# Performance work log

Measured on AMD Instinct MI355X. Metric: run time of the kernel, lower is better.

The kernel has to match this reference:

```python
import jax, jax.numpy as jnp
import numpy as np
from jax import lax

R = 3                      # blob_r
S = 2 * R + 1              # 7: maxpool / neighborhood kernel size
THRESH = 0.997
PS_XY = 0.1                # vs_xy
PS_Z = 0.02                # vs_z
ZMIN = -2.0                # zrange[0]
K_PEAKS = 131072           # static upper bound replacing torch.nonzero

_offs = np.arange(S)
_gz, _gy, _gx = np.meshgrid(_offs, _offs, _offs, indexing='ij')  # patch axis order [z,y,x]
GZ = jnp.asarray(_gz.ravel(), dtype=jnp.int32)
GY = jnp.asarray(_gy.ravel(), dtype=jnp.int32)
GX = jnp.asarray(_gx.ravel(), dtype=jnp.int32)
# centroid filters: offsets -r..r along the matching patch axis (matches torch meshgrid layout)
FZ = jnp.asarray((_gz.ravel() - R).astype(np.float32))
FY = jnp.asarray((_gy.ravel() - R).astype(np.float32))
FX = jnp.asarray((_gx.ravel() - R).astype(np.float32))


def setup_inputs() -> dict:
    key = jax.random.key(0)
    pred_vol = jax.random.uniform(key, (1, 1, 128, 512, 512), dtype=jnp.float32)
    return {"pred_vol": pred_vol, "max_peaks": K_PEAKS}


def _forward(pred_vol, max_peaks):
    vol = pred_vol[0, 0]                               # [D,H,W]
    D, H, W = vol.shape
    thr = jnp.where(vol > THRESH, vol, 0.0)
    # MaxPool3d(kernel=2r+1, stride=1, padding=r) == SAME max window (pad with -inf)
    mp = lax.reduce_window(thr, -jnp.inf, lax.max, (S, S, S), (1, 1, 1), [(R, R)] * 3)
    conf = jnp.where((mp > 0.0) & (mp == thr), mp, 0.0)  # local maxima above threshold
    # fixed-size peak extraction (replaces torch.nonzero); zero-valued entries are padding
    vals, idx = lax.top_k(conf.reshape(-1), max_peaks)   # [K], [K]
    z = idx // (H * W)
    y = (idx % (H * W)) // W
    x = idx % W
    padv = jnp.pad(vol, R)                               # ConstantPad3d(r, 0)
    # gather (2r+1)^3 neighborhoods around each peak: [K, S^3]
    patches = padv[z[:, None] + GZ[None, :], y[:, None] + GY[None, :], x[:, None] + GX[None, :]]
    s0 = patches.sum(axis=1)                             # conv3d with ones filter == conf_rec sum
    xloc = jnp.einsum('kp,p->k', patches, FX) / s0
    yloc = jnp.einsum('kp,p->k', patches, FY) / s0
    zloc = jnp.einsum('kp,p->k', patches, FZ) / s0
    xf = x.astype(jnp.float32)
    yf = y.astype(jnp.float32)
    zf = z.astype(jnp.float32)
    xrec = (xf + xloc - (W - 1) / 2.0) * PS_XY
    yrec = (yf + yloc - (H - 1) / 2.0) * PS_XY
    zrec = (zf + zloc + 0.5) * PS_Z + ZMIN
    valid = vals > 0.0
    xyz = jnp.where(valid[:, None], jnp.stack((xrec, yrec, zrec), axis=1), 0.0)  # [K,3]
    out = jnp.concatenate([xyz, vals[:, None]], axis=1)  # [K,4] = (x,y,z,conf), padded rows are 0
    return out, valid


def reference(pred_vol, max_peaks):
    return _forward(pred_vol, max_peaks)
```

## Files before the change

### kernel.cpp

```cpp
#include <hip/hip_runtime.h>

#define DD 128
#define HH 512
#define WW 512
#define NVOX (DD*HH*WW)
#define THRESHV 0.997f
#define KPEAKS 131072
#define PEAK_CAP (1u<<18)
#define NBINS 65536


__global__ void k_init(unsigned* counters, unsigned* hist) {
    unsigned t = blockIdx.x * 1024u + threadIdx.x;
    if (t < 64) counters[t] = 0u;
    if (t < NBINS) hist[t] = 0u;
}

__global__ __launch_bounds__(512, 4)
void k_find(const float4* __restrict__ vol4, const float* __restrict__ vol,
            unsigned* counters, unsigned* hist,
            unsigned long long* keys, float4* psums) {
    __shared__ float4 tile[2][2048];
    __shared__ unsigned lcnt, pcnt, lbase;
    __shared__ unsigned cidx[384];
    __shared__ unsigned long long lbuf[192];
    __shared__ float4 sbuf[192];
    if (threadIdx.x == 0) { lcnt = 0; pcnt = 0; }
    __syncthreads();

    unsigned t = threadIdx.x;
    unsigned lane = t & 63u;
    unsigned w = t >> 6;
    unsigned blockBase4 = blockIdx.x * 4096u;
    int dz = (int)lane / 7, dy = (int)lane - dz * 7;

    auto dma = [&](unsigned s) {
#pragma unroll
        for (unsigned i = 0; i < 4; i++) {
            unsigned f = i * 512u + w * 64u;
            const float4* gp = vol4 + blockBase4 + s * 2048u + f + lane;
            __builtin_amdgcn_global_load_lds(
                (const __attribute__((address_space(1))) unsigned int*)gp,
                (__attribute__((address_space(3))) unsigned int*)(&tile[s][f]),
                16, 0, 0);
        }
    };

    auto scan = [&](unsigned s) {
        unsigned m = 0u;
        float4 v[4];
#pragma unroll
        for (unsigned i = 0; i < 4; i++) v[i] = tile[s][i * 512u + t];
#pragma unroll
        for (unsigned i = 0; i < 4; i++) {
            m |= (v[i].x > THRESHV ? 1u : 0u) << (4 * i);
            m |= (v[i].y > THRESHV ? 1u : 0u) << (4 * i + 1);
            m |= (v[i].z > THRESHV ? 1u : 0u) << (4 * i + 2);
            m |= (v[i].w > THRESHV ? 1u : 0u) << (4 * i + 3);
        }
        unsigned sbase4 = blockBase4 + s * 2048u;
        while (m) {
            int b = __ffs(m) - 1;
            m &= m - 1u;
            unsigned f4 = sbase4 + (unsigned)(b >> 2) * 512u + t;
            cidx[atomicAdd(&lcnt, 1u) & 383u] = f4 * 4u + (unsigned)(b & 3);
        }
    };

    auto verify = [&](unsigned n) {
        for (unsigned base = w * 2u; base < n; base += 16u) {
            bool has2 = (base + 1u < n);
            unsigned idxA = cidx[base];
            unsigned idxB = has2 ? cidx[base + 1u] : idxA;
            int zA = idxA >> 18, yA = (idxA >> 9) & 511, xA = idxA & 511;
            int zB = idxB >> 18, yB = (idxB >> 9) & 511, xB = idxB & 511;
            int nzA = zA + dz - 3, nyA = yA + dy - 3;
            int nzB = zB + dz - 3, nyB = yB + dy - 3;
            bool rowokA = (lane < 49) && ((unsigned)nzA < DD) && ((unsigned)nyA < HH);
            bool rowokB = (lane < 49) && ((unsigned)nzB < DD) && ((unsigned)nyB < HH);
            size_t rbA = rowokA ? (((size_t)(unsigned)nzA << 18) | ((size_t)(unsigned)nyA << 9))
                                : (((size_t)zA << 18) | ((size_t)yA << 9));
            size_t rbB = rowokB ? (((size_t)(unsigned)nzB << 18) | ((size_t)(unsigned)nyB << 9))
                                : (((size_t)zB << 18) | ((size_t)yB << 9));
            float rvA[7], rvB[7];
            bool intAB = (xA >= 3) && (xA <= WW - 4) && (xB >= 3) && (xB <= WW - 4);
            if (intAB) {
                float4 fA0 = *(const float4*)(vol + rbA + (unsigned)(xA - 3));
                float4 fA1 = *(const float4*)(vol + rbA + (unsigned)(xA + 1));
                float4 fB0 = *(const float4*)(vol + rbB + (unsigned)(xB - 3));
                float4 fB1 = *(const float4*)(vol + rbB + (unsigned)(xB + 1));
                rvA[0] = fA0.x; rvA[1] = fA0.y; rvA[2] = fA0.z; rvA[3] = fA0.w;
                rvA[4] = fA1.x; rvA[5] = fA1.y; rvA[6] = fA1.z;
                rvB[0] = fB0.x; rvB[1] = fB0.y; rvB[2] = fB0.z; rvB[3] = fB0.w;
                rvB[4] = fB1.x; rvB[5] = fB1.y; rvB[6] = fB1.z;
            } else {
#pragma unroll
                for (int d = 0; d < 7; d++) {
                    int nxA = xA + d - 3;
                    bool okA = (unsigned)nxA < WW;
                    float va = vol[rbA + (unsigned)(okA ? nxA : xA)];
                    rvA[d] = okA ? va : 0.f;
                    int nxB = xB + d - 3;
                    bool okB = (unsigned)nxB < WW;
                    float vb = vol[rbB + (unsigned)(okB ? nxB : xB)];
                    rvB[d] = okB ? vb : 0.f;
                }
            }
            if (!rowokA) {
#pragma unroll
                for (int d = 0; d < 7; d++) rvA[d] = 0.f;
            }
            if (!rowokB) {
#pragma unroll
                for (int d = 0; d < 7; d++) rvB[d] = 0.f;
            }
            float centerA = __shfl(rvA[3], 24);
            float centerB = __shfl(rvB[3], 24);

            {
                bool kill = false;
                float s0r = 0.f, sxr = 0.f;
#pragma unroll
                for (int d = 0; d < 7; d++) {
                    kill |= rvA[d] > centerA;
                    s0r += rvA[d];
                    sxr += rvA[d] * (float)(d - 3);
                }
                if (!__any(kill)) {
                    float s0 = s0r, sx = sxr;
                    float sy = s0r * (float)(dy - 3);
                    float sz = s0r * (float)(dz - 3);
                    for (int off = 32; off; off >>= 1) {
                        s0 += __shfl_down(s0, off);
                        sx += __shfl_down(sx, off);
                        sy += __shfl_down(sy, off);
                        sz += __shfl_down(sz, off);
                    }
                    if (lane == 0) {
                        unsigned bits = __float_as_uint(centerA);
                        atomicAdd(&hist[(~bits) & 0xFFFFu], 1u);
                        unsigned li = atomicAdd(&pcnt, 1u);
                        if (li < 192u) {
                            lbuf[li] = ((unsigned long long)bits << 32) | idxA;
                            sbuf[li] = make_float4(s0, sx, sy, sz);
                        }
                    }
                }
            }
            if (has2) {
                bool kill = false;
                float s0r = 0.f, sxr = 0.f;
#pragma unroll
                for (int d = 0; d < 7; d++) {
                    kill |= rvB[d] > centerB;
                    s0r += rvB[d];
                    sxr += rvB[d] * (float)(d - 3);
                }
                if (!__any(kill)) {
                    float s0 = s0r, sx = sxr;
                    float sy = s0r * (float)(dy - 3);
                    float sz = s0r * (float)(dz - 3);
                    for (int off = 32; off; off >>= 1) {
                        s0 += __shfl_down(s0, off);
                        sx += __shfl_down(sx, off);
                        sy += __shfl_down(sy, off);
                        sz += __shfl_down(sz, off);
                    }
                    if (lane == 0) {
                        unsigned bits = __float_as_uint(centerB);
                        atomicAdd(&hist[(~bits) & 0xFFFFu], 1u);
                        unsigned li = atomicAdd(&pcnt, 1u);
                        if (li < 192u) {
                            lbuf[li] = ((unsigned long long)bits << 32) | idxB;
                            sbuf[li] = make_float4(s0, sx, sy, sz);
                        }
                    }
                }
            }
        }
    };

    dma(0u);
    __builtin_amdgcn_s_waitcnt(0);
    __syncthreads();
    scan(0u);
    __syncthreads();
    unsigned n0 = lcnt > 384u ? 384u : lcnt;

    dma(1u);
    verify(n0);
    __syncthreads();
    if (t == 0) lcnt = 0;
    __syncthreads();

    scan(1u);
    __syncthreads();
    unsigned n1 = lcnt > 384u ? 384u : lcnt;
    verify(n1);

    __syncthreads();
    if (threadIdx.x == 0) lbase = atomicAdd(&counters[1], pcnt);
    __syncthreads();
    unsigned np = pcnt > 192u ? 192u : pcnt;
    for (unsigned i = threadIdx.x; i < np; i += 512u) {
        unsigned p = lbase + i;
        if (p < PEAK_CAP) { keys[p] = lbuf[i]; psums[p] = sbuf[i]; }
    }
}

__global__ void k_scan_a(const unsigned* __restrict__ hist,
                         unsigned* __restrict__ cursor,
                         unsigned* __restrict__ blocksum) {
    __shared__ unsigned sc[256];
    unsigned t = threadIdx.x, b = blockIdx.x;
    unsigned h = hist[b * 256u + t];
    sc[t] = h;
    __syncthreads();
    for (unsigned off = 1u; off < 256u; off <<= 1) {
        unsigned v = (t >= off) ? sc[t - off] : 0u;
        __syncthreads();
        sc[t] += v;
        __syncthreads();
    }
    cursor[b * 256u + t] = sc[t] - h;
    if (t == 255u) blocksum[b] = sc[255];
}

__global__ void k_scatter(const unsigned* __restrict__ counters,
                          const unsigned long long* __restrict__ keys,
                          const unsigned* __restrict__ blocksum,
                          unsigned* cursor, unsigned long long* sorted,
                          unsigned* sslot,
                          float4* __restrict__ out, float* __restrict__ valid) {
    __shared__ unsigned bs[256];
    unsigned t = threadIdx.x;
    if (t < 256u) bs[t] = blocksum[t];
    __syncthreads();
    for (unsigned off = 1u; off < 256u; off <<= 1) {
        unsigned v = (t < 256u && t >= off) ? bs[t - off] : 0u;
        __syncthreads();
        if (t < 256u) bs[t] += v;
        __syncthreads();
    }
    unsigned np = counters[1]; if (np > PEAK_CAP) np = PEAK_CAP;
    unsigned g = blockIdx.x * 1024u + t;
    if (g < np) {
        unsigned long long key = keys[g];
        unsigned bits = (unsigned)(key >> 32);
        unsigned bin = (~bits) & 0xFFFFu;
        unsigned c = bin >> 8;
        unsigned base_c = (c > 0u) ? bs[c - 1u] : 0u;
        unsigned pos = base_c + atomicAdd(&cursor[bin], 1u);
        if (pos < PEAK_CAP) { sorted[pos] = key; sslot[pos] = g; }
    } else if (g < KPEAKS) {
        out[g] = make_float4(0.f, 0.f, 0.f, 0.f);
        valid[g] = 0.f;
    }
}

__global__ void k_finish(const unsigned* __restrict__ counters,
                         const unsigned long long* __restrict__ sorted,
                         const unsigned* __restrict__ sslot,
                         const float4* __restrict__ psums,
                         float4* __restrict__ out, float* __restrict__ valid) {
    unsigned np = counters[1]; if (np > PEAK_CAP) np = PEAK_CAP;
    unsigned t = blockIdx.x * 1024u + threadIdx.x;
    if (t >= np) return;
    unsigned long long key = sorted[t];
    unsigned bits = (unsigned)(key >> 32);
    unsigned s = t;
    while (s > 0 && (unsigned)(sorted[s - 1] >> 32) == bits) s--;
    unsigned myidx = (unsigned)key;
    unsigned rank = 0, e = s;
    while (e < np) {
        unsigned long long k2 = sorted[e];
        if ((unsigned)(k2 >> 32) != bits) break;
        if ((unsigned)k2 < myidx) rank++;
        e++;
    }
    unsigned row = s + rank;
    if (row >= KPEAKS) return;
    unsigned idx = myidx;
    int z = idx >> 18, y = (idx >> 9) & 511, x = idx & 511;
    float4 ps = psums[sslot[t]];
    float val = __uint_as_float(bits);
    float xloc = ps.y / ps.x, yloc = ps.z / ps.x, zloc = ps.w / ps.x;
    float xr = ((float)x + xloc - (float)(WW - 1) * 0.5f) * 0.1f;
    float yr = ((float)y + yloc - (float)(HH - 1) * 0.5f) * 0.1f;
    float zr = ((float)z + zloc + 0.5f) * 0.02f - 2.0f;
    out[row] = make_float4(xr, yr, zr, val);
    valid[row] = 1.f;
}

extern "C" void kernel_launch(void* const* d_in, const int* in_sizes, int n_in,
                              void* d_out, int out_size, void* d_ws, size_t ws_size,
                              hipStream_t stream) {
    const float* vol = (const float*)d_in[0];

    char* w = (char*)d_ws;
    unsigned* counters = (unsigned*)w;
    unsigned* hist     = (unsigned*)(w + 1024);
    unsigned* cursor   = (unsigned*)(w + 1024 + NBINS * 4);
    char* w2 = w + 1024 + 2 * NBINS * 4;
    unsigned long long* keys   = (unsigned long long*)w2;
    unsigned long long* sorted = keys + PEAK_CAP;
    unsigned* sslot = (unsigned*)(sorted + PEAK_CAP);
    float4*   psums = (float4*)(sslot + PEAK_CAP);
    unsigned* blocksum = (unsigned*)(psums + PEAK_CAP);

    float* out_rows = (float*)d_out;
    float* valid = out_rows + (size_t)KPEAKS * 4;

    k_init<<<NBINS / 1024, 1024, 0, stream>>>(counters, hist);
    k_find<<<NVOX / 16384, 512, 0, stream>>>((const float4*)vol, vol, counters, hist, keys, psums);
    k_scan_a<<<256, 256, 0, stream>>>(hist, cursor, blocksum);
    k_scatter<<<PEAK_CAP / 1024, 1024, 0, stream>>>(counters, keys, blocksum, cursor,
                                                    sorted, sslot,
                                                    (float4*)out_rows, valid);
    k_finish<<<PEAK_CAP / 1024, 1024, 0, stream>>>(counters, sorted, sslot, psums,
                                                   (float4*)out_rows, valid);
}
```

Measured before the change: 252.6 us.

## Replace double-buffered LDS DMA with direct register loads, halve block work

k_find no longer copies the volume into a 64KB double-buffered LDS tile with global_load_lds. Each thread now loads its four float4 values straight into registers. Each block covers half as many voxels, so the grid doubles and launch bounds go from 4 to 8 blocks per CU. This drops the LDS footprint and the staging synchronisation so more waves are resident to hide memory latency, but it gives up the overlap between the second tile's DMA and the first tile's verify pass.

```diff
diff --git a/kernel.cpp b/kernel.cpp
--- a/kernel.cpp
+++ b/kernel.cpp
@@ -16,11 +16,10 @@
     if (t < NBINS) hist[t] = 0u;
 }
 
-__global__ __launch_bounds__(512, 4)
+__global__ __launch_bounds__(512, 8)
 void k_find(const float4* __restrict__ vol4, const float* __restrict__ vol,
             unsigned* counters, unsigned* hist,
             unsigned long long* keys, float4* psums) {
-    __shared__ float4 tile[2][2048];
     __shared__ unsigned lcnt, pcnt, lbase;
     __shared__ unsigned cidx[384];
     __shared__ unsigned long long lbuf[192];
@@ -31,173 +30,151 @@
     unsigned t = threadIdx.x;
     unsigned lane = t & 63u;
     unsigned w = t >> 6;
-    unsigned blockBase4 = blockIdx.x * 4096u;
+    unsigned blockBase4 = blockIdx.x * 2048u;
+
+    unsigned b4 = blockBase4 + t;
+    float4 a0 = vol4[b4];
+    float4 a1 = vol4[b4 + 512u];
+    float4 a2 = vol4[b4 + 1024u];
+    float4 a3 = vol4[b4 + 1536u];
+    __builtin_amdgcn_sched_barrier(0);
+    unsigned m = 0u;
+    m |= (a0.x > THRESHV ? 1u : 0u);
+    m |= (a0.y > THRESHV ? 2u : 0u);
+    m |= (a0.z > THRESHV ? 4u : 0u);
+    m |= (a0.w > THRESHV ? 8u : 0u);
+    m |= (a1.x > THRESHV ? 16u : 0u);
+    m |= (a1.y > THRESHV ? 32u : 0u);
+    m |= (a1.z > THRESHV ? 64u : 0u);
+    m |= (a1.w > THRESHV ? 128u : 0u);
+    m |= (a2.x > THRESHV ? 256u : 0u);
+    m |= (a2.y > THRESHV ? 512u : 0u);
+    m |= (a2.z > THRESHV ? 1024u : 0u);
+    m |= (a2.w > THRESHV ? 2048u : 0u);
+    m |= (a3.x > THRESHV ? 4096u : 0u);
+    m |= (a3.y > THRESHV ? 8192u : 0u);
+    m |= (a3.z > THRESHV ? 16384u : 0u);
+    m |= (a3.w > THRESHV ? 32768u : 0u);
+    while (m) {
+        int b = __ffs(m) - 1;
+        m &= m - 1u;
+        unsigned f4 = blockBase4 + (unsigned)(b >> 2) * 512u + t;
+        cidx[atomicAdd(&lcnt, 1u) & 383u] = f4 * 4u + (unsigned)(b & 3);
+    }
+    __syncthreads();
+
+    unsigned n = lcnt > 384u ? 384u : lcnt;
     int dz = (int)lane / 7, dy = (int)lane - dz * 7;
-
-    auto dma = [&](unsigned s) {
-#pragma unroll
-        for (unsigned i = 0; i < 4; i++) {
-            unsigned f = i * 512u + w * 64u;
-            const float4* gp = vol4 + blockBase4 + s * 2048u + f + lane;
-            __builtin_amdgcn_global_load_lds(
-                (const __attribute__((address_space(1))) unsigned int*)gp,
-                (__attribute__((address_space(3))) unsigned int*)(&tile[s][f]),
-                16, 0, 0);
-        }
-    };
-
-    auto scan = [&](unsigned s) {
-        unsigned m = 0u;
-        float4 v[4];
-#pragma unroll
-        for (unsigned i = 0; i < 4; i++) v[i] = tile[s][i * 512u + t];
-#pragma unroll
-        for (unsigned i = 0; i < 4; i++) {
-            m |= (v[i].x > THRESHV ? 1u : 0u) << (4 * i);
-            m |= (v[i].y > THRESHV ? 1u : 0u) << (4 * i + 1);
-            m |= (v[i].z > THRESHV ? 1u : 0u) << (4 * i + 2);
-            m |= (v[i].w > THRESHV ? 1u : 0u) << (4 * i + 3);
-        }
-        unsigned sbase4 = blockBase4 + s * 2048u;
-        while (m) {
-            int b = __ffs(m) - 1;
-            m &= m - 1u;
-            unsigned f4 = sbase4 + (unsigned)(b >> 2) * 512u + t;
-            cidx[atomicAdd(&lcnt, 1u) & 383u] = f4 * 4u + (unsigned)(b & 3);
-        }
-    };
-
-    auto verify = [&](unsigned n) {
-        for (unsigned base = w * 2u; base < n; base += 16u) {
-            bool has2 = (base + 1u < n);
-            unsigned idxA = cidx[base];
-            unsigned idxB = has2 ? cidx[base + 1u] : idxA;
-            int zA = idxA >> 18, yA = (idxA >> 9) & 511, xA = idxA & 511;
-            int zB = idxB >> 18, yB = (idxB >> 9) & 511, xB = idxB & 511;
-            int nzA = zA + dz - 3, nyA = yA + dy - 3;
-            int nzB = zB + dz - 3, nyB = yB + dy - 3;
-            bool rowokA = (lane < 49) && ((unsigned)nzA < DD) && ((unsigned)nyA < HH);
-            bool rowokB = (lane < 49) && ((unsigned)nzB < DD) && ((unsigned)nyB < HH);
-            size_t rbA = rowokA ? (((size_t)(unsigned)nzA << 18) | ((size_t)(unsigned)nyA << 9))
-                                : (((size_t)zA << 18) | ((size_t)yA << 9));
-            size_t rbB = rowokB ? (((size_t)(unsigned)nzB << 18) | ((size_t)(unsigned)nyB << 9))
-                                : (((size_t)zB << 18) | ((size_t)yB << 9));
-            float rvA[7], rvB[7];
-            bool intAB = (xA >= 3) && (xA <= WW - 4) && (xB >= 3) && (xB <= WW - 4);
-            if (intAB) {
-                float4 fA0 = *(const float4*)(vol + rbA + (unsigned)(xA - 3));
-                float4 fA1 = *(const float4*)(vol + rbA + (unsigned)(xA + 1));
-                float4 fB0 = *(const float4*)(vol + rbB + (unsigned)(xB - 3));
-                float4 fB1 = *(const float4*)(vol + rbB + (unsigned)(xB + 1));
-                rvA[0] = fA0.x; rvA[1] = fA0.y; rvA[2] = fA0.z; rvA[3] = fA0.w;
-                rvA[4] = fA1.x; rvA[5] = fA1.y; rvA[6] = fA1.z;
-                rvB[0] = fB0.x; rvB[1] = fB0.y; rvB[2] = fB0.z; rvB[3] = fB0.w;
-                rvB[4] = fB1.x; rvB[5] = fB1.y; rvB[6] = fB1.z;
-            } else {
-#pragma unroll
-                for (int d = 0; d < 7; d++) {
-                    int nxA = xA + d - 3;
-                    bool okA = (unsigned)nxA < WW;
-                    float va = vol[rbA + (unsigned)(okA ? nxA : xA)];
-                    rvA[d] = okA ? va : 0.f;
-                    int nxB = xB + d - 3;
-                    bool okB = (unsigned)nxB < WW;
-                    float vb = vol[rbB + (unsigned)(okB ? nxB : xB)];
-                    rvB[d] = okB ? vb : 0.f;
-                }
-            }
-            if (!rowokA) {
-#pragma unroll
-                for (int d = 0; d < 7; d++) rvA[d] = 0.f;
-            }
-            if (!rowokB) {
-#pragma unroll
-                for (int d = 0; d < 7; d++) rvB[d] = 0.f;
-            }
-            float centerA = __shfl(rvA[3], 24);
-            float centerB = __shfl(rvB[3], 24);
-
-            {
-                bool kill = false;
-                float s0r = 0.f, sxr = 0.f;
-#pragma unroll
-                for (int d = 0; d < 7; d++) {
-                    kill |= rvA[d] > centerA;
-                    s0r += rvA[d];
-                    sxr += rvA[d] * (float)(d - 3);
-                }
-                if (!__any(kill)) {
-                    float s0 = s0r, sx = sxr;
-                    float sy = s0r * (float)(dy - 3);
-                    float sz = s0r * (float)(dz - 3);
-                    for (int off = 32; off; off >>= 1) {
-                        s0 += __shfl_down(s0, off);
-                        sx += __shfl_down(sx, off);
-                        sy += __shfl_down(sy, off);
-                        sz += __shfl_down(sz, off);
+    for (unsigned base = w * 2u; base < n; base += 16u) {
+        bool has2 = (base + 1u < n);
+        unsigned idxA = cidx[base];
+        unsigned idxB = has2 ? cidx[base + 1u] : idxA;
+        int zA = idxA >> 18, yA = (idxA >> 9) & 511, xA = idxA & 511;
+        int zB = idxB >> 18, yB = (idxB >> 9) & 511, xB = idxB & 511;
+        int nzA = zA + dz - 3, nyA = yA + dy - 3;
+        int nzB = zB + dz - 3, nyB = yB + dy - 3;
+        bool rowokA = (lane < 49) && ((unsigned)nzA < DD) && ((unsigned)nyA < HH);
+        bool rowokB = (lane < 49) && ((unsigned)nzB < DD) && ((unsigned)nyB < HH);
+        size_t rbA = rowokA ? (((size_t)(unsigned)nzA << 18) | ((size_t)(unsigned)nyA << 9))
+                            : (((size_t)zA << 18) | ((size_t)yA << 9));
+        size_t rbB = rowokB ? (((size_t)(unsigned)nzB << 18) | ((size_t)(unsigned)nyB << 9))
+                            : (((size_t)zB << 18) | ((size_t)yB << 9));
+        float rvA[7], rvB[7];
+        bool intAB = (xA >= 3) && (xA <= WW - 4) && (xB >= 3) && (xB <= WW - 4);
+        if (intAB) {
+            float4 fA0 = *(const float4*)(vol + rbA + (unsigned)(xA - 3));
+            float4 fA1 = *(const float4*)(vol + rbA + (unsigned)(xA + 1));
+            float4 fB0 = *(const float4*)(vol + rbB + (unsigned)(xB - 3));
+            float4 fB1 = *(const float4*)(vol + rbB + (unsigned)(xB + 1));
+            rvA[0] = fA0.x; rvA[1] = fA0.y; rvA[2] = fA0.z; rvA[3] = fA0.w;
+            rvA[4] = fA1.x; rvA[5] = fA1.y; rvA[6] = fA1.z;
+            rvB[0] = fB0.x; rvB[1] = fB0.y; rvB[2] = fB0.z; rvB[3] = fB0.w;
+            rvB[4] = fB1.x; rvB[5] = fB1.y; rvB[6] = fB1.z;
+        } else {
+#pragma unroll
+            for (int d = 0; d < 7; d++) {
+                int nxA = xA + d - 3;
+                bool okA = (unsigned)nxA < WW;
+                float va = vol[rbA + (unsigned)(okA ? nxA : xA)];
+                rvA[d] = okA ? va : 0.f;
+                int nxB = xB + d - 3;
+                bool okB = (unsigned)nxB < WW;
+                float vb = vol[rbB + (unsigned)(okB ? nxB : xB)];
+                rvB[d] = okB ? vb : 0.f;
+            }
+        }
+        if (!rowokA) {
+#pragma unroll
+            for (int d = 0; d < 7; d++) rvA[d] = 0.f;
+        }
+        if (!rowokB) {
+#pragma unroll
+            for (int d = 0; d < 7; d++) rvB[d] = 0.f;
+        }
+        float centerA = __shfl(rvA[3], 24);
+        float centerB = __shfl(rvB[3], 24);
+
+        {
+            bool kill = false;
+            float s0r = 0.f, sxr = 0.f;
+#pragma unroll
+            for (int d = 0; d < 7; d++) {
+                kill |= rvA[d] > centerA;
+                s0r += rvA[d];
+                sxr += rvA[d] * (float)(d - 3);
+            }
+            if (!__any(kill)) {
+                float s0 = s0r, sx = sxr;
+                float sy = s0r * (float)(dy - 3);
+                float sz = s0r * (float)(dz - 3);
+                for (int off = 32; off; off >>= 1) {
+                    s0 += __shfl_down(s0, off);
+                    sx += __shfl_down(sx, off);
+                    sy += __shfl_down(sy, off);
+                    sz += __shfl_down(sz, off);
+                }
+                if (lane == 0) {
+                    unsigned bits = __float_as_uint(centerA);
+                    atomicAdd(&hist[(~bits) & 0xFFFFu], 1u);
+                    unsigned li = atomicAdd(&pcnt, 1u);
+                    if (li < 192u) {
+                        lbuf[li] = ((unsigned long long)bits << 32) | idxA;
+                        sbuf[li] = make_float4(s0, sx, sy, sz);
                     }
-                    if (lane == 0) {
-                        unsigned bits = __float_as_uint(centerA);
-                        atomicAdd(&hist[(~bits) & 0xFFFFu], 1u);
-                        unsigned li = atomicAdd(&pcnt, 1u);
-                        if (li < 192u) {
-                            lbuf[li] = ((unsigned long long)bits << 32) | idxA;
-                            sbuf[li] = make_float4(s0, sx, sy, sz);
-                        }
+                }
+            }
+        }
+        if (has2) {
+            bool kill = false;
+            float s0r = 0.f, sxr = 0.f;
+#pragma unroll
+            for (int d = 0; d < 7; d++) {
+                kill |= rvB[d] > centerB;
+                s0r += rvB[d];
+                sxr += rvB[d] * (float)(d - 3);
+            }
+            if (!__any(kill)) {
+                float s0 = s0r, sx = sxr;
+                float sy = s0r * (float)(dy - 3);
+                float sz = s0r * (float)(dz - 3);
+                for (int off = 32; off; off >>= 1) {
+                    s0 += __shfl_down(s0, off);
+                    sx += __shfl_down(sx, off);
+                    sy += __shfl_down(sy, off);
+                    sz += __shfl_down(sz, off);
+                }
+                if (lane == 0) {
+                    unsigned bits = __float_as_uint(centerB);
+                    atomicAdd(&hist[(~bits) & 0xFFFFu], 1u);
+                    unsigned li = atomicAdd(&pcnt, 1u);
+                    if (li < 192u) {
+                        lbuf[li] = ((unsigned long long)bits << 32) | idxB;
+                        sbuf[li] = make_float4(s0, sx, sy, sz);
                     }
                 }
             }
-            if (has2) {
-                bool kill = false;
-                float s0r = 0.f, sxr = 0.f;
-#pragma unroll
-                for (int d = 0; d < 7; d++) {
-                    kill |= rvB[d] > centerB;
-                    s0r += rvB[d];
-                    sxr += rvB[d] * (float)(d - 3);
-                }
-                if (!__any(kill)) {
-                    float s0 = s0r, sx = sxr;
-                    float sy = s0r * (float)(dy - 3);
-                    float sz = s0r * (float)(dz - 3);
-                    for (int off = 32; off; off >>= 1) {
-                        s0 += __shfl_down(s0, off);
-                        sx += __shfl_down(sx, off);
-                        sy += __shfl_down(sy, off);
-                        sz += __shfl_down(sz, off);
-                    }
-                    if (lane == 0) {
-                        unsigned bits = __float_as_uint(centerB);
-                        atomicAdd(&hist[(~bits) & 0xFFFFu], 1u);
-                        unsigned li = atomicAdd(&pcnt, 1u);
-                        if (li < 192u) {
-                            lbuf[li] = ((unsigned long long)bits << 32) | idxB;
-                            sbuf[li] = make_float4(s0, sx, sy, sz);
-                        }
-                    }
-                }
-            }
-        }
-    };
-
-    dma(0u);
-    __builtin_amdgcn_s_waitcnt(0);
-    __syncthreads();
-    scan(0u);
-    __syncthreads();
-    unsigned n0 = lcnt > 384u ? 384u : lcnt;
-
-    dma(1u);
-    verify(n0);
-    __syncthreads();
-    if (t == 0) lcnt = 0;
-    __syncthreads();
-
-    scan(1u);
-    __syncthreads();
-    unsigned n1 = lcnt > 384u ? 384u : lcnt;
-    verify(n1);
-
+        }
+    }
     __syncthreads();
     if (threadIdx.x == 0) lbase = atomicAdd(&counters[1], pcnt);
     __syncthreads();
@@ -312,7 +289,7 @@
     float* valid = out_rows + (size_t)KPEAKS * 4;
 
     k_init<<<NBINS / 1024, 1024, 0, stream>>>(counters, hist);
-    k_find<<<NVOX / 16384, 512, 0, stream>>>((const float4*)vol, vol, counters, hist, keys, psums);
+    k_find<<<NVOX / 8192, 512, 0, stream>>>((const float4*)vol, vol, counters, hist, keys, psums);
     k_scan_a<<<256, 256, 0, stream>>>(hist, cursor, blocksum);
     k_scatter<<<PEAK_CAP / 1024, 1024, 0, stream>>>(counters, keys, blocksum, cursor,
                                                     sorted, sslot,
```

Result: faster. 241.9 us (-4.2%).
